# Optimization experiments

Measured on AMD Instinct MI355X. Metric: run time of the kernel, lower is better.

## Reference

```python
import jax, jax.numpy as jnp
import numpy as np
from jax import lax

B, T, F, D, K = 64, 1000, 140, 256, 7
TAU, V_TH, EPS, ALPHA = 2.0, 1.0, 1e-5, 2.0
PAD = (K - 1) // 2

# Heaviside spike with ATan surrogate gradient (spikingjelly default, alpha=2)
@jax.custom_vjp
def spike_fn(x):
    return (x >= 0.0).astype(x.dtype)

def _spike_fwd(x):
    return spike_fn(x), x

def _spike_bwd(x, g):
    sg = (ALPHA / 2.0) / (1.0 + (jnp.pi / 2.0 * ALPHA * x) ** 2)
    return (g * sg,)

spike_fn.defvjp(_spike_fwd, _spike_bwd)

def lif(x_seq):
    """Multi-step LIF: v += (x - v)/tau, hard reset to 0 on spike. x_seq: (T,B,D)."""
    def step(v, x):
        v = v + (x - v) / TAU
        s = spike_fn(v - V_TH)
        return v * (1.0 - s), s
    _, spikes = lax.scan(step, jnp.zeros_like(x_seq[0]), x_seq)
    return spikes

def bn(x, g, b, m, v):
    # eval-mode BatchNorm1d over channel dim D (last axis of (T,B,D))
    return (x - m) * (g * lax.rsqrt(v + EPS)) + b

def setup_inputs() -> dict:
    key = jax.random.key(0)
    ks = jax.random.split(key, 4)
    s = 0.05
    return {
        "x": jax.random.normal(ks[0], (B, T, F), jnp.float32),
        "pw_w": jax.random.normal(ks[1], (D, F), jnp.float32) * s,
        "pw_b": jnp.zeros((D,), jnp.float32),
        "dw_w": jax.random.normal(ks[2], (D, 1, K), jnp.float32) * s,  # depthwise (O,I/g,K)
        "bn1_g": jnp.ones((D,), jnp.float32),
        "bn1_b": jnp.zeros((D,), jnp.float32),
        "bn1_m": jnp.zeros((D,), jnp.float32),
        "bn1_v": jnp.ones((D,), jnp.float32),
        "lin_w": jax.random.normal(ks[3], (D, D), jnp.float32) * s,
        "bn2_g": jnp.ones((D,), jnp.float32),
        "bn2_b": jnp.zeros((D,), jnp.float32),
        "bn2_m": jnp.zeros((D,), jnp.float32),
        "bn2_v": jnp.ones((D,), jnp.float32),
    }

def reference(x, pw_w, pw_b, dw_w, bn1_g, bn1_b, bn1_m, bn1_v,
              lin_w, bn2_g, bn2_b, bn2_m, bn2_v):
    # pointwise conv: (B,T,F) -> (B,D,T)
    h = jnp.einsum('btf,df->bdt', x, pw_w) + pw_b[None, :, None]
    # depthwise temporal conv, groups=D, same padding
    h = lax.conv_general_dilated(h, dw_w, window_strides=(1,),
                                 padding=[(PAD, PAD)], feature_group_count=D,
                                 dimension_numbers=('NCH', 'OIH', 'NCH'))
    h = jnp.transpose(h, (2, 0, 1))  # (T,B,D) multi-step layout
    h = lif(bn(h, bn1_g, bn1_b, bn1_m, bn1_v))
    residual = h
    h = jnp.einsum('tbd,ed->tbe', h, lin_w)
    h = lif(bn(h, bn2_g, bn2_b, bn2_m, bn2_v))
    return h + residual
```

## Files before the change

### kernel.cpp

```cpp
#include <hip/hip_runtime.h>
#include <hip/hip_bf16.h>

#define B_  64
#define T_  1000
#define F_  140
#define D_  256
#define EPS_ 1e-5f

#define CL_ 50
#define NC_ 20
#define W_  24

#define CW3_ 34
#define NCH3_ 30
#define HST3_ 268
#define AST_ 168

typedef __attribute__((ext_vector_type(8))) short bf16x8;
typedef __attribute__((ext_vector_type(4))) short bf16x4;
typedef __attribute__((ext_vector_type(4))) float f32x4;
typedef unsigned long long u64;

static __device__ inline short f2bf(float f) {
  __hip_bfloat16 h = __float2bfloat16(f);
  return *reinterpret_cast<short*>(&h);
}
static __device__ inline float bf2f(short s) {
  unsigned int u = ((unsigned int)(unsigned short)s) << 16;
  return __uint_as_float(u);
}

__global__ __launch_bounds__(256) void k0_prep(const float* __restrict__ lw,
                                               float* __restrict__ lwT,
                                               const float* __restrict__ pw,
                                               short* __restrict__ wfrag) {
  int i = blockIdx.x * 256 + threadIdx.x;
  if (i < 65536) {
    int e = i >> 8, d = i & 255;
    lwT[(size_t)d * D_ + e] = lw[(size_t)e * D_ + d];
  } else if (i < 65536 + 40960) {
    int j = i - 65536;
    int q = j & 7;
    int lane = (j >> 3) & 63;
    int rest = j >> 9;
    int kk = rest % 5, ntile = rest / 5;
    int n = ntile * 16 + (lane & 15);
    int k = kk * 32 + (lane >> 4) * 8 + q;
    wfrag[j] = (k < F_) ? f2bf(pw[(size_t)n * F_ + k]) : (short)0;
  }
}

__global__ __launch_bounds__(256) void k12_fused(const float* __restrict__ x,
                                                 const short* __restrict__ wfrag,
                                                 const float* __restrict__ bias,
                                                 const float* __restrict__ dww,
                                                 const float* __restrict__ g1,
                                                 const float* __restrict__ b1,
                                                 const float* __restrict__ m1,
                                                 const float* __restrict__ v1,
                                                 u64* __restrict__ bits) {
  __shared__ short smem[64 * HST3_];
  short* Abuf = smem;
  short* hbuf = smem;
  const int b = blockIdx.x;
  const int c = blockIdx.y;
  const int tb = CW3_ * c - 27;
  const int tid = threadIdx.x;
  const int lane = tid & 63, wv = tid >> 6;
  const int lr = lane & 15, quad = lane >> 4;

  {
    const int arow = tid >> 2, aseg = tid & 3;
    const int ak0 = aseg * 36;
    const int anum4 = (aseg == 3) ? 8 : 9;
    const int ta = tb + arow;
    short* adst = Abuf + arow * AST_ + ak0;
    if (ta >= 0 && ta < T_) {
      const float* xrow = x + ((size_t)b * T_ + ta) * F_ + ak0;
#pragma unroll
      for (int q = 0; q < 9; q++) {
        if (q < anum4) {
          float4 av = *(const float4*)(xrow + q * 4);
          bf16x4 pk = {f2bf(av.x), f2bf(av.y), f2bf(av.z), f2bf(av.w)};
          *(bf16x4*)(adst + q * 4) = pk;
        }
      }
    } else {
      bf16x4 z = {0, 0, 0, 0};
#pragma unroll
      for (int q = 0; q < 9; q++)
        if (q < anum4) *(bf16x4*)(adst + q * 4) = z;
    }
    if (aseg == 3) {
      bf16x4 z = {0, 0, 0, 0};
#pragma unroll
      for (int q = 0; q < 5; q++) *(bf16x4*)(adst + 32 + q * 4) = z;
    }
  }
  __syncthreads();

  f32x4 acc[4][4] = {};
  const short* wfb = wfrag + (size_t)(wv * 4 * 5) * 512 + lane * 8;
#pragma unroll
  for (int kk = 0; kk < 5; kk++) {
    bf16x8 bfr[4], af[4];
#pragma unroll
    for (int j = 0; j < 4; j++)
      bfr[j] = *(const bf16x8*)(wfb + (size_t)(j * 5 + kk) * 512);
#pragma unroll
    for (int i = 0; i < 4; i++)
      af[i] = *(const bf16x8*)(Abuf + (i * 16 + lr) * AST_ + kk * 32 + quad * 8);
#pragma unroll
    for (int i = 0; i < 4; i++)
#pragma unroll
      for (int j = 0; j < 4; j++)
        acc[i][j] = __builtin_amdgcn_mfma_f32_16x16x32_bf16(af[i], bfr[j], acc[i][j], 0, 0, 0);
  }
  __syncthreads();

#pragma unroll
  for (int j = 0; j < 4; j++) {
    const int n = wv * 64 + j * 16 + lr;
    const float badd = bias[n];
#pragma unroll
    for (int i = 0; i < 4; i++) {
#pragma unroll
      for (int r = 0; r < 4; r++) {
        const int row = i * 16 + quad * 4 + r;
        const int t = tb + row;
        short val = (t >= 0 && t < T_) ? f2bf(acc[i][j][r] + badd) : (short)0;
        hbuf[row * HST3_ + n] = val;
      }
    }
  }
  __syncthreads();

  {
    const int d = tid;
    const float scv = g1[d] * rsqrtf(v1[d] + EPS_);
    float w2[7];
#pragma unroll
    for (int k = 0; k < 7; k++) w2[k] = dww[d * 7 + k] * (0.5f * scv);
    const float sh2 = 0.5f * (b1[d] - m1[d] * scv);

    const int wb = (c == 0) ? 24 : 0;
    float win0 = bf2f(hbuf[(wb + 0) * HST3_ + d]);
    float win1 = bf2f(hbuf[(wb + 1) * HST3_ + d]);
    float win2 = bf2f(hbuf[(wb + 2) * HST3_ + d]);
    float win3 = bf2f(hbuf[(wb + 3) * HST3_ + d]);
    float win4 = bf2f(hbuf[(wb + 4) * HST3_ + d]);
    float win5 = bf2f(hbuf[(wb + 5) * HST3_ + d]);
    float v = 0.f;

    if (c != 0) {
#pragma unroll
      for (int s0 = 0; s0 < 24; s0 += 8) {
        float tap[8];
#pragma unroll
        for (int g = 0; g < 8; g++) tap[g] = bf2f(hbuf[(s0 + g + 6) * HST3_ + d]);
#pragma unroll
        for (int g = 0; g < 8; g++) {
          float u2 = win0 * w2[0] + win1 * w2[1] + win2 * w2[2] + win3 * w2[3] +
                     win4 * w2[4] + win5 * w2[5] + tap[g] * w2[6] + sh2;
          v = 0.5f * v + u2;
          v = (v >= 1.0f) ? 0.f : v;
          win0 = win1; win1 = win2; win2 = win3; win3 = win4; win4 = win5; win5 = tap[g];
        }
      }
    }
    const int tw0 = CW3_ * c;
    const int smax = T_ - tw0;
    u64* bp = bits + ((size_t)b * T_ + tw0) * 4 + wv;
    const bool lane0 = (lane == 0);
#pragma unroll
    for (int s0 = 0; s0 < 32; s0 += 8) {
      float tap[8];
#pragma unroll
      for (int g = 0; g < 8; g++) tap[g] = bf2f(hbuf[(s0 + g + 30) * HST3_ + d]);
#pragma unroll
      for (int g = 0; g < 8; g++) {
        float u2 = win0 * w2[0] + win1 * w2[1] + win2 * w2[2] + win3 * w2[3] +
                   win4 * w2[4] + win5 * w2[5] + tap[g] * w2[6] + sh2;
        v = 0.5f * v + u2;
        bool sp = (v >= 1.0f);
        u64 mask = __ballot(sp);
        if (lane0 && (s0 + g) < smax) bp[(size_t)(s0 + g) * 4] = mask;
        v = sp ? 0.f : v;
        win0 = win1; win1 = win2; win2 = win3; win3 = win4; win4 = win5; win5 = tap[g];
      }
    }
    {
      float tap[2];
#pragma unroll
      for (int g = 0; g < 2; g++) tap[g] = bf2f(hbuf[(32 + g + 30) * HST3_ + d]);
#pragma unroll
      for (int g = 0; g < 2; g++) {
        float u2 = win0 * w2[0] + win1 * w2[1] + win2 * w2[2] + win3 * w2[3] +
                   win4 * w2[4] + win5 * w2[5] + tap[g] * w2[6] + sh2;
        v = 0.5f * v + u2;
        bool sp = (v >= 1.0f);
        u64 mask = __ballot(sp);
        if (lane0 && (32 + g) < smax) bp[(size_t)(32 + g) * 4] = mask;
        v = sp ? 0.f : v;
        win0 = win1; win1 = win2; win2 = win3; win3 = win4; win4 = win5; win5 = tap[g];
      }
    }
  }
}

__global__ __launch_bounds__(256) void k3_lin_lif(const u64* __restrict__ bits,
                                                  const float* __restrict__ lwT,
                                                  const float* __restrict__ g2,
                                                  const float* __restrict__ b2,
                                                  const float* __restrict__ m2,
                                                  const float* __restrict__ v2,
                                                  float* __restrict__ out) {
  __shared__ u64 sb[(CL_ + W_) * 4];
  const int b = blockIdx.x;
  const int t0 = blockIdx.y * CL_;
  const int tstart = (t0 >= W_) ? t0 - W_ : 0;
  const int nwarm = t0 - tstart;
  const int nsteps = nwarm + CL_;
  const int e = threadIdx.x;
  const u64* gbp = bits + ((size_t)b * T_ + tstart) * 4;
  for (int i = e; i < nsteps * 4; i += 256) sb[i] = gbp[i];
  __syncthreads();

  const float sc = g2[e] * rsqrtf(v2[e] + EPS_);
  const float shf = b2[e] - m2[e] * sc;
  const int eq = e >> 6, eb = e & 63;
  float v = 0.f;

  if (nwarm) {
#pragma unroll
    for (int s0 = 0; s0 < 24; s0 += 4) {
      u64 a0[4], a1[4], a2[4], a3[4];
#pragma unroll
      for (int g = 0; g < 4; g++) {
        a0[g] = sb[(s0 + g) * 4 + 0]; a1[g] = sb[(s0 + g) * 4 + 1];
        a2[g] = sb[(s0 + g) * 4 + 2]; a3[g] = sb[(s0 + g) * 4 + 3];
      }
#pragma unroll
      for (int g = 0; g < 4; g++) {
        float u = shf;
        if (a0[g] | a1[g] | a2[g] | a3[g]) {
          float acc = 0.f;
          u64 mm;
          mm = a0[g]; while (mm) { int l = __builtin_ctzll(mm); mm &= mm - 1; acc += lwT[(size_t)(l) * D_ + e]; }
          mm = a1[g]; while (mm) { int l = __builtin_ctzll(mm); mm &= mm - 1; acc += lwT[(size_t)(64 + l) * D_ + e]; }
          mm = a2[g]; while (mm) { int l = __builtin_ctzll(mm); mm &= mm - 1; acc += lwT[(size_t)(128 + l) * D_ + e]; }
          mm = a3[g]; while (mm) { int l = __builtin_ctzll(mm); mm &= mm - 1; acc += lwT[(size_t)(192 + l) * D_ + e]; }
          u = acc * sc + shf;
        }
        v = 0.5f * (v + u);
        v = (v >= 1.0f) ? 0.f : v;
      }
    }
  }
  float* op = out + ((size_t)t0 * B_ + b) * D_ + e;
  const size_t ts = (size_t)B_ * D_;
#pragma unroll
  for (int s0 = 0; s0 < 50; s0 += 5) {
    u64 a0[5], a1[5], a2[5], a3[5];
#pragma unroll
    for (int g = 0; g < 5; g++) {
      const int s = nwarm + s0 + g;
      a0[g] = sb[s * 4 + 0]; a1[g] = sb[s * 4 + 1];
      a2[g] = sb[s * 4 + 2]; a3[g] = sb[s * 4 + 3];
    }
#pragma unroll
    for (int g = 0; g < 5; g++) {
      float u = shf;
      if (a0[g] | a1[g] | a2[g] | a3[g]) {
        float acc = 0.f;
        u64 mm;
        mm = a0[g]; while (mm) { int l = __builtin_ctzll(mm); mm &= mm - 1; acc += lwT[(size_t)(l) * D_ + e]; }
        mm = a1[g]; while (mm) { int l = __builtin_ctzll(mm); mm &= mm - 1; acc += lwT[(size_t)(64 + l) * D_ + e]; }
        mm = a2[g]; while (mm) { int l = __builtin_ctzll(mm); mm &= mm - 1; acc += lwT[(size_t)(128 + l) * D_ + e]; }
        mm = a3[g]; while (mm) { int l = __builtin_ctzll(mm); mm &= mm - 1; acc += lwT[(size_t)(192 + l) * D_ + e]; }
        u = acc * sc + shf;
      }
      v = 0.5f * (v + u);
      bool sp = (v >= 1.0f);
      u64 myw = (eq == 0) ? a0[g] : (eq == 1) ? a1[g] : (eq == 2) ? a2[g] : a3[g];
      float s1 = (float)((myw >> eb) & 1ull);
      op[(size_t)(s0 + g) * ts] = (sp ? 1.0f : 0.0f) + s1;
      v = sp ? 0.f : v;
    }
  }
}

extern "C" void kernel_launch(void* const* d_in, const int* in_sizes, int n_in,
                              void* d_out, int out_size, void* d_ws, size_t ws_size,
                              hipStream_t stream) {
  const float* x    = (const float*)d_in[0];
  const float* pw_w = (const float*)d_in[1];
  const float* pw_b = (const float*)d_in[2];
  const float* dw_w = (const float*)d_in[3];
  const float* g1   = (const float*)d_in[4];
  const float* b1   = (const float*)d_in[5];
  const float* m1   = (const float*)d_in[6];
  const float* v1   = (const float*)d_in[7];
  const float* lw   = (const float*)d_in[8];
  const float* g2   = (const float*)d_in[9];
  const float* b2   = (const float*)d_in[10];
  const float* m2   = (const float*)d_in[11];
  const float* v2   = (const float*)d_in[12];
  float* out = (float*)d_out;

  char* ws = (char*)d_ws;
  u64* bits = (u64*)ws;
  float* lwT = (float*)(ws + 2048000);
  short* wfrag = (short*)(ws + 2048000 + 262144);

  k0_prep<<<(65536 + 40960 + 255) / 256, 256, 0, stream>>>(lw, lwT, pw_w, wfrag);
  dim3 g_k12(B_, NCH3_);
  k12_fused<<<g_k12, 256, 0, stream>>>(x, wfrag, pw_b, dw_w, g1, b1, m1, v1, bits);
  dim3 g_k3(B_, NC_);
  k3_lin_lif<<<g_k3, 256, 0, stream>>>(bits, lwT, g2, b2, m2, v2, out);
}
```

Baseline: 160.4 us.

## Split fused conv+LIF kernel into conv-to-buffer and separate LIF scan

The fused pointwise+depthwise+LIF kernel used 30 chunks of 34 steps, each recomputing a 27-row halo (24 LIF warm-up steps plus conv padding) through the matmul. It now computes the pre-activation u once per 58-step chunk with only a 6-row conv halo and writes it to global memory in bf16 (T,B,D) layout. A new kernel then reloads u in 40-step chunks with 24-step warm-up and runs the LIF scan to emit spike bitmasks. This removes redundant matmul work on the warm-up rows but adds an extra kernel launch and a roughly 32 MB bf16 round trip through global memory.

```diff
diff --git a/kernel.cpp b/kernel.cpp
--- a/kernel.cpp
+++ b/kernel.cpp
@@ -11,10 +11,13 @@
 #define NC_ 20
 #define W_  24
 
-#define CW3_ 34
-#define NCH3_ 30
+#define CV_  58
+#define NCV_ 18
 #define HST3_ 268
 #define AST_ 168
+
+#define SCL_ 40
+#define SNC_ 25
 
 typedef __attribute__((ext_vector_type(8))) short bf16x8;
 typedef __attribute__((ext_vector_type(4))) short bf16x4;
@@ -50,21 +53,21 @@
   }
 }
 
-__global__ __launch_bounds__(256) void k12_fused(const float* __restrict__ x,
-                                                 const short* __restrict__ wfrag,
-                                                 const float* __restrict__ bias,
-                                                 const float* __restrict__ dww,
-                                                 const float* __restrict__ g1,
-                                                 const float* __restrict__ b1,
-                                                 const float* __restrict__ m1,
-                                                 const float* __restrict__ v1,
-                                                 u64* __restrict__ bits) {
+__global__ __launch_bounds__(256) void k1u(const float* __restrict__ x,
+                                           const short* __restrict__ wfrag,
+                                           const float* __restrict__ bias,
+                                           const float* __restrict__ dww,
+                                           const float* __restrict__ g1,
+                                           const float* __restrict__ b1,
+                                           const float* __restrict__ m1,
+                                           const float* __restrict__ v1,
+                                           short* __restrict__ u) {
   __shared__ short smem[64 * HST3_];
   short* Abuf = smem;
   short* hbuf = smem;
   const int b = blockIdx.x;
   const int c = blockIdx.y;
-  const int tb = CW3_ * c - 27;
+  const int tb = CV_ * c - 3;
   const int tid = threadIdx.x;
   const int lane = tid & 63, wv = tid >> 6;
   const int lr = lane & 15, quad = lane >> 4;
@@ -143,67 +146,89 @@
     for (int k = 0; k < 7; k++) w2[k] = dww[d * 7 + k] * (0.5f * scv);
     const float sh2 = 0.5f * (b1[d] - m1[d] * scv);
 
-    const int wb = (c == 0) ? 24 : 0;
-    float win0 = bf2f(hbuf[(wb + 0) * HST3_ + d]);
-    float win1 = bf2f(hbuf[(wb + 1) * HST3_ + d]);
-    float win2 = bf2f(hbuf[(wb + 2) * HST3_ + d]);
-    float win3 = bf2f(hbuf[(wb + 3) * HST3_ + d]);
-    float win4 = bf2f(hbuf[(wb + 4) * HST3_ + d]);
-    float win5 = bf2f(hbuf[(wb + 5) * HST3_ + d]);
-    float v = 0.f;
-
-    if (c != 0) {
-#pragma unroll
-      for (int s0 = 0; s0 < 24; s0 += 8) {
-        float tap[8];
-#pragma unroll
-        for (int g = 0; g < 8; g++) tap[g] = bf2f(hbuf[(s0 + g + 6) * HST3_ + d]);
-#pragma unroll
-        for (int g = 0; g < 8; g++) {
-          float u2 = win0 * w2[0] + win1 * w2[1] + win2 * w2[2] + win3 * w2[3] +
-                     win4 * w2[4] + win5 * w2[5] + tap[g] * w2[6] + sh2;
-          v = 0.5f * v + u2;
-          v = (v >= 1.0f) ? 0.f : v;
-          win0 = win1; win1 = win2; win2 = win3; win3 = win4; win4 = win5; win5 = tap[g];
+    float win0 = bf2f(hbuf[0 * HST3_ + d]);
+    float win1 = bf2f(hbuf[1 * HST3_ + d]);
+    float win2 = bf2f(hbuf[2 * HST3_ + d]);
+    float win3 = bf2f(hbuf[3 * HST3_ + d]);
+    float win4 = bf2f(hbuf[4 * HST3_ + d]);
+    float win5 = bf2f(hbuf[5 * HST3_ + d]);
+#pragma unroll
+    for (int r = 0; r < CV_; r++) {
+      float tap = bf2f(hbuf[(r + 6) * HST3_ + d]);
+      float uh = win0 * w2[0] + win1 * w2[1] + win2 * w2[2] + win3 * w2[3] +
+                 win4 * w2[4] + win5 * w2[5] + tap * w2[6] + sh2;
+      hbuf[r * HST3_ + d] = f2bf(uh);
+      win0 = win1; win1 = win2; win2 = win3; win3 = win4; win4 = win5; win5 = tap;
+    }
+  }
+  __syncthreads();
+
+  {
+    const int t0 = CV_ * c;
+#pragma unroll
+    for (int ii = 0; ii < 8; ii++) {
+      const int i = tid + ii * 256;
+      if (i < CV_ * 32) {
+        const int r = i >> 5, v8 = i & 31;
+        const int t = t0 + r;
+        if (t < T_) {
+          *(bf16x8*)(u + ((size_t)t * B_ + b) * D_ + v8 * 8) =
+              *(const bf16x8*)(hbuf + r * HST3_ + v8 * 8);
         }
       }
     }
-    const int tw0 = CW3_ * c;
-    const int smax = T_ - tw0;
-    u64* bp = bits + ((size_t)b * T_ + tw0) * 4 + wv;
-    const bool lane0 = (lane == 0);
-#pragma unroll
-    for (int s0 = 0; s0 < 32; s0 += 8) {
-      float tap[8];
-#pragma unroll
-      for (int g = 0; g < 8; g++) tap[g] = bf2f(hbuf[(s0 + g + 30) * HST3_ + d]);
-#pragma unroll
-      for (int g = 0; g < 8; g++) {
-        float u2 = win0 * w2[0] + win1 * w2[1] + win2 * w2[2] + win3 * w2[3] +
-                   win4 * w2[4] + win5 * w2[5] + tap[g] * w2[6] + sh2;
-        v = 0.5f * v + u2;
-        bool sp = (v >= 1.0f);
-        u64 mask = __ballot(sp);
-        if (lane0 && (s0 + g) < smax) bp[(size_t)(s0 + g) * 4] = mask;
-        v = sp ? 0.f : v;
-        win0 = win1; win1 = win2; win2 = win3; win3 = win4; win4 = win5; win5 = tap[g];
-      }
-    }
-    {
-      float tap[2];
-#pragma unroll
-      for (int g = 0; g < 2; g++) tap[g] = bf2f(hbuf[(32 + g + 30) * HST3_ + d]);
-#pragma unroll
-      for (int g = 0; g < 2; g++) {
-        float u2 = win0 * w2[0] + win1 * w2[1] + win2 * w2[2] + win3 * w2[3] +
-                   win4 * w2[4] + win5 * w2[5] + tap[g] * w2[6] + sh2;
-        v = 0.5f * v + u2;
-        bool sp = (v >= 1.0f);
-        u64 mask = __ballot(sp);
-        if (lane0 && (32 + g) < smax) bp[(size_t)(32 + g) * 4] = mask;
-        v = sp ? 0.f : v;
-        win0 = win1; win1 = win2; win2 = win3; win3 = win4; win4 = win5; win5 = tap[g];
-      }
+  }
+}
+
+__global__ __launch_bounds__(256) void k2s(const short* __restrict__ u,
+                                           u64* __restrict__ bits) {
+  __shared__ short uls[64 * D_];
+  const int b = blockIdx.x;
+  const int t0 = blockIdx.y * SCL_;
+  const int tid = threadIdx.x;
+
+  {
+#pragma unroll
+    for (int ii = 0; ii < 8; ii++) {
+      const int i = tid + ii * 256;
+      const int r = i >> 5, v8 = i & 31;
+      const int t = t0 - W_ + r;
+      bf16x8 val = {0, 0, 0, 0, 0, 0, 0, 0};
+      if (t >= 0 && t < T_)
+        val = *(const bf16x8*)(u + ((size_t)t * B_ + b) * D_ + v8 * 8);
+      *(bf16x8*)(uls + r * D_ + v8 * 8) = val;
+    }
+  }
+  __syncthreads();
+
+  const int d = tid;
+  const int lane = tid & 63, wv = tid >> 6;
+  float v = 0.f;
+#pragma unroll
+  for (int s0 = 0; s0 < W_; s0 += 8) {
+    float tap[8];
+#pragma unroll
+    for (int g = 0; g < 8; g++) tap[g] = bf2f(uls[(s0 + g) * D_ + d]);
+#pragma unroll
+    for (int g = 0; g < 8; g++) {
+      v = 0.5f * v + tap[g];
+      v = (v >= 1.0f) ? 0.f : v;
+    }
+  }
+  u64* bp = bits + ((size_t)b * T_ + t0) * 4 + wv;
+  const bool lane0 = (lane == 0);
+#pragma unroll
+  for (int s0 = 0; s0 < SCL_; s0 += 8) {
+    float tap[8];
+#pragma unroll
+    for (int g = 0; g < 8; g++) tap[g] = bf2f(uls[(W_ + s0 + g) * D_ + d]);
+#pragma unroll
+    for (int g = 0; g < 8; g++) {
+      v = 0.5f * v + tap[g];
+      bool sp = (v >= 1.0f);
+      u64 mask = __ballot(sp);
+      if (lane0) bp[(size_t)(s0 + g) * 4] = mask;
+      v = sp ? 0.f : v;
     }
   }
 }
@@ -309,13 +334,16 @@
   float* out = (float*)d_out;
 
   char* ws = (char*)d_ws;
-  u64* bits = (u64*)ws;
-  float* lwT = (float*)(ws + 2048000);
-  short* wfrag = (short*)(ws + 2048000 + 262144);
+  short* u = (short*)ws;
+  u64* bits = (u64*)(ws + 32768000);
+  float* lwT = (float*)(ws + 32768000 + 2048000);
+  short* wfrag = (short*)(ws + 32768000 + 2048000 + 262144);
 
   k0_prep<<<(65536 + 40960 + 255) / 256, 256, 0, stream>>>(lw, lwT, pw_w, wfrag);
-  dim3 g_k12(B_, NCH3_);
-  k12_fused<<<g_k12, 256, 0, stream>>>(x, wfrag, pw_b, dw_w, g1, b1, m1, v1, bits);
+  dim3 g_k1(B_, NCV_);
+  k1u<<<g_k1, 256, 0, stream>>>(x, wfrag, pw_b, dw_w, g1, b1, m1, v1, u);
+  dim3 g_k2(B_, SNC_);
+  k2s<<<g_k2, 256, 0, stream>>>(u, bits);
   dim3 g_k3(B_, NC_);
   k3_lin_lif<<<g_k3, 256, 0, stream>>>(bits, lwT, g2, b2, m2, v2, out);
 }
```

Result: slower. 167.6 us (+4.5%).
